# Performance work log

Measured on AMD Instinct MI355X. Metric: run time of the kernel, lower is better.

## Reference

```python
import jax, jax.numpy as jnp
import numpy as np

C = 2.3026  # Poincare ball curvature
EPS = 1e-15

def _hlinear(x, z, r, c):
    # hypll-style Poincare fully connected layer (HNN++, Shimizu et al.)
    # x: (B, fi) on ball, z: (fi, fo), r: (fo,)
    cs = jnp.sqrt(c)
    lam = 2.0 / (1.0 - c * jnp.sum(x * x, axis=-1, keepdims=True))  # conformal factor (B,1)
    zn = jnp.maximum(jnp.sqrt(jnp.sum(z * z, axis=0)), EPS)         # (fo,)
    tcr = 2.0 * cs * r                                              # (fo,)
    # signed hyperplane distances v_k
    d = (2.0 * zn / cs) * jnp.arcsinh(
        cs * lam * (x @ z) / zn * jnp.cosh(tcr) - (lam - 1.0) * jnp.sinh(tcr))
    w = jnp.sinh(cs * d) / cs
    # map back into the ball: ||out|| < 1/sqrt(c)
    return w / (1.0 + jnp.sqrt(1.0 + c * jnp.sum(w * w, axis=-1, keepdims=True)))

def _hrelu(x, c):
    # logmap at origin -> ReLU in tangent space -> expmap at origin
    cs = jnp.sqrt(c)
    n = jnp.maximum(jnp.sqrt(jnp.sum(x * x, axis=-1, keepdims=True)), EPS)
    v = jnp.arctanh(jnp.minimum(cs * n, 1.0 - 1e-7)) * x / (cs * n)
    v = jax.nn.relu(v)
    vn = jnp.maximum(jnp.sqrt(jnp.sum(v * v, axis=-1, keepdims=True)), EPS)
    return jnp.tanh(cs * vn) * v / (cs * vn)

def setup_inputs() -> dict:
    key = jax.random.key(0)
    ks = jax.random.split(key, 9)
    B, D = 65536, 768
    xs = 0.02 * jax.random.normal(ks[0], (B, D), dtype=jnp.float32)
    # repo preprocessing: lift to Lorentz (K=C) then Lorentz->Poincare
    x0 = jnp.sqrt(1.0 / C + jnp.sum(xs * xs, axis=-1, keepdims=True))
    x = xs / (x0 + 1.0)  # strictly inside ball of radius 1/sqrt(C)
    def mk(k, fi, fo):
        return (jax.random.normal(k, (fi, fo), dtype=jnp.float32) / np.float32(np.sqrt(fi)))
    return {
        "x": x,
        "z1": mk(ks[1], 768, 512), "b1": 0.01 * jax.random.normal(ks[2], (512,), dtype=jnp.float32),
        "z2": mk(ks[3], 512, 256), "b2": 0.01 * jax.random.normal(ks[4], (256,), dtype=jnp.float32),
        "z3": mk(ks[5], 256, 128), "b3": 0.01 * jax.random.normal(ks[6], (128,), dtype=jnp.float32),
        "z4": mk(ks[7], 128, 1),   "b4": 0.01 * jax.random.normal(ks[8], (1,), dtype=jnp.float32),
    }

def reference(x, z1, b1, z2, b2, z3, b3, z4, b4):
    h = _hrelu(_hlinear(x, z1, b1, C), C)
    h = _hrelu(_hlinear(h, z2, b2, C), C)
    h = _hrelu(_hlinear(h, z3, b3, C), C)
    return _hlinear(h, z4, b4, C)
```

## Files before the change

### kernel.cpp

```cpp
#include <hip/hip_runtime.h>

#define CURV 2.3026f
#define EPSF 1e-15f

typedef __attribute__((ext_vector_type(8))) short bfrag8;
typedef __attribute__((ext_vector_type(4))) float ffrag4;

__device__ __forceinline__ unsigned short f2bf(float f) {
  unsigned u = __builtin_bit_cast(unsigned, f);
  u += 0x7fffu + ((u >> 16) & 1u);
  return (unsigned short)(u >> 16);
}

__device__ __forceinline__ void gld16(const void* g, void* l) {
  unsigned lo = (unsigned)(unsigned long long)l;
  __builtin_amdgcn_global_load_lds(
      (const __attribute__((address_space(1))) unsigned int*)g,
      (__attribute__((address_space(3))) unsigned int*)lo, 16, 0, 0);
}

__global__ __launch_bounds__(256) void xprep(const float* __restrict__ x,
                                             unsigned short* __restrict__ xb,
                                             float* __restrict__ lam0) {
  const int t = threadIdx.x, lane = t & 63, w = t >> 6;
  const long row = (long)blockIdx.x * 4 + w;
  const float* xr = x + row * 768;
  unsigned short* xo = xb + row * 768;
  float ss = 0.f;
#pragma unroll
  for (int j = 0; j < 3; j++) {
    float4 v = *(const float4*)(xr + 4 * (lane + 64 * j));
    ss += v.x * v.x + v.y * v.y + v.z * v.z + v.w * v.w;
    ushort4 b; b.x = f2bf(v.x); b.y = f2bf(v.y); b.z = f2bf(v.z); b.w = f2bf(v.w);
    *(ushort4*)(xo + 4 * (lane + 64 * j)) = b;
  }
#pragma unroll
  for (int m = 1; m <= 32; m <<= 1) ss += __shfl_xor(ss, m);
  if (lane == 0) lam0[row] = 2.f / (1.f - CURV * ss);
}

__global__ void prep_weights(const float* __restrict__ z, const float* __restrict__ r,
                             unsigned short* __restrict__ zT, float* __restrict__ stats,
                             int K, int N) {
  int n = blockIdx.x, t = threadIdx.x;
  float ss = 0.f;
  for (int k = t; k < K; k += 128) {
    float v = z[(size_t)k * N + n];
    ss += v * v;
    zT[(size_t)n * K + k] = f2bf(v);
  }
  __shared__ float red[128];
  red[t] = ss; __syncthreads();
  for (int s = 64; s > 0; s >>= 1) { if (t < s) red[t] += red[t + s]; __syncthreads(); }
  if (t == 0) {
    float zn = fmaxf(sqrtf(red[0]), EPSF);
    float cs = sqrtf(CURV);
    float tc = 2.f * cs * r[n];
    stats[4*n+0] = 2.f * (zn - 1.f);
    stats[4*n+1] = coshf(tc) / zn;
    stats[4*n+2] = sinhf(tc);
    stats[4*n+3] = 0.f;
  }
}

template<int K, int N, bool LAST>
__launch_bounds__(512, 2)
__global__ void hlayer(const unsigned short* __restrict__ Ain,
                       const unsigned short* __restrict__ zT,
                       const float* __restrict__ stats,
                       const float* __restrict__ lamIn,
                       unsigned short* __restrict__ Hout,
                       float* __restrict__ lamOut,
                       const float* __restrict__ z4,
                       const float* __restrict__ st4,
                       float* __restrict__ outF) {
  constexpr int NT = N / 64;
  constexpr int KI = K / 32;
  constexpr int NBW = N / 128;
  constexpr int BUF = 4096 + N * 64;
  constexpr int HSB = LAST ? 0 : 64 * (N + 8) * 2;
  constexpr int SM = (2 * BUF > HSB) ? 2 * BUF : HSB;
  __shared__ __align__(16) char smem[SM];
  __shared__ float lamS[64];
  __shared__ float gamS[64];
  __shared__ float sums[3][64];

  const int t = threadIdx.x;
  const int wid = t >> 6, lane = t & 63;
  const int wm = wid >> 2, wn = wid & 3;
  const int lm = lane & 15, quad = lane >> 4;
  const int l7 = lane & 7, rl8 = lane >> 3;
  const unsigned rowg0 = blockIdx.x * 64;

  const char* Abase = (const char*)Ain;
  const char* Bbase = (const char*)zT;
  unsigned aoff = 0, aLds = 0;
  if (wid < 4) {
    unsigned R = 8 * wid + rl8;
    unsigned c = l7 ^ rl8;
    unsigned m = 2 * R + (c >> 2);
    aoff = (rowg0 + m) * (unsigned)(K * 2) + (c & 3) * 16;
    aLds = wid * 1024 + lane * 16;
  }
  unsigned boff[NBW], bLds[NBW];
#pragma unroll
  for (int j = 0; j < NBW; j++) {
    unsigned R = 8 * (wid + 8 * j) + rl8;
    unsigned c = l7 ^ rl8;
    unsigned n = 2 * R + (c >> 2);
    boff[j] = n * (unsigned)(K * 2) + (c & 3) * 16;
    bLds[j] = (wid + 8 * j) * 1024 + lane * 16;
  }

  const unsigned sl16 = ((((lm & 1) << 2) + quad) ^ (lm >> 1)) << 4;
  unsigned afoff[2], bfoff[NT];
#pragma unroll
  for (int tm = 0; tm < 2; tm++)
    afoff[tm] = (16 * wm + 8 * tm + (lm >> 1)) * 128 + sl16;
#pragma unroll
  for (int tn = 0; tn < NT; tn++)
    bfoff[tn] = 4096 + (wn * (N / 8) + 8 * tn + (lm >> 1)) * 128 + sl16;

  {
    char* buf = smem;
    if (wid < 4) gld16(Abase + aoff, buf + aLds);
#pragma unroll
    for (int j = 0; j < NBW; j++) gld16(Bbase + boff[j], buf + 4096 + bLds[j]);
  }

  ffrag4 acc[2][NT];
#pragma unroll
  for (int a = 0; a < 2; a++)
#pragma unroll
    for (int b = 0; b < NT; b++) acc[a][b] = (ffrag4){0.f, 0.f, 0.f, 0.f};

  for (int k = 0; k < KI; k++) {
    __syncthreads();
    char* cur = smem + (k & 1) * BUF;
    char* nxt = smem + ((k + 1) & 1) * BUF;
    if (k + 1 < KI) {
      unsigned adv = (unsigned)(k + 1) * 64;
      if (wid < 4) gld16(Abase + aoff + adv, nxt + aLds);
#pragma unroll
      for (int j = 0; j < NBW; j++) gld16(Bbase + boff[j] + adv, nxt + 4096 + bLds[j]);
    }
    bfrag8 af0 = *(const bfrag8*)(cur + afoff[0]);
    bfrag8 af1 = *(const bfrag8*)(cur + afoff[1]);
#pragma unroll
    for (int tn = 0; tn < NT; tn++) {
      bfrag8 bf = *(const bfrag8*)(cur + bfoff[tn]);
      acc[0][tn] = __builtin_amdgcn_mfma_f32_16x16x32_bf16(af0, bf, acc[0][tn], 0, 0, 0);
      acc[1][tn] = __builtin_amdgcn_mfma_f32_16x16x32_bf16(af1, bf, acc[1][tn], 0, 0, 0);
    }
  }

  if (t < 64) {
    sums[0][t] = 0.f; sums[1][t] = 0.f; sums[2][t] = 0.f;
    lamS[t] = lamIn[rowg0 + t];
  }
  float z4v[NT];
  if (LAST) {
#pragma unroll
    for (int tn = 0; tn < NT; tn++) z4v[tn] = z4[wn * (N / 4) + 16 * tn + lm];
  }
  __syncthreads();

  const float cs = sqrtf(CURV), inv_cs = 1.f / cs;

#pragma unroll
  for (int tn = 0; tn < NT; tn++) {
    float4 st = *(const float4*)(stats + 4 * (wn * (N / 4) + 16 * tn + lm));
    float dl = st.x, chozn = st.y, sh = st.z;
#pragma unroll
    for (int tm = 0; tm < 2; tm++) {
#pragma unroll
      for (int rg = 0; rg < 4; rg++) {
        float lam = lamS[32 * wm + 16 * tm + 4 * quad + rg];
        float g = cs * lam * acc[tm][tn][rg] * chozn - (lam - 1.f) * sh;
        float q = g * g;
        float u = g * (1.f - q * (1.f / 6.f) + q * q * 0.075f - q * q * q * 0.044642857f);
        float d1 = dl * u;
        float S = 2.f * g * sqrtf(1.f + q);
        float Ch = 1.f + 2.f * q;
        acc[tm][tn][rg] = (S * (1.f + 0.5f * d1 * d1) + Ch * d1) * inv_cs;
      }
    }
  }
#pragma unroll
  for (int tm = 0; tm < 2; tm++) {
#pragma unroll
    for (int rg = 0; rg < 4; rg++) {
      float s2 = 0.f, sp2 = 0.f, s4 = 0.f;
#pragma unroll
      for (int tn = 0; tn < NT; tn++) {
        float w = acc[tm][tn][rg];
        s2 += w * w;
        float wp = fmaxf(w, 0.f);
        sp2 += wp * wp;
        if (LAST) s4 += wp * z4v[tn];
      }
#pragma unroll
      for (int m = 1; m <= 8; m <<= 1) {
        s2 += __shfl_xor(s2, m, 16);
        sp2 += __shfl_xor(sp2, m, 16);
        if (LAST) s4 += __shfl_xor(s4, m, 16);
      }
      if (lm == 0) {
        int row = 32 * wm + 16 * tm + 4 * quad + rg;
        atomicAdd(&sums[0][row], s2);
        atomicAdd(&sums[1][row], sp2);
        if (LAST) atomicAdd(&sums[2][row], s4);
      }
    }
  }
  __syncthreads();
  if (t < 64) {
    float sw2 = sums[0][t], swp2 = sums[1][t];
    float den = 1.f + sqrtf(1.f + CURV * sw2);
    float nn = fmaxf(sqrtf(sw2) / den, EPSF);
    float al = atanhf(fminf(cs * nn, 1.f - 1e-7f)) / (cs * nn);
    float vn = fmaxf(al * sqrtf(swp2) / den, EPSF);
    float be = tanhf(cs * vn) / (cs * vn);
    float gam = al * be / den;
    if (LAST) {
      float s = gam * sums[2][t];
      float lamh = 2.f / (1.f - CURV * gam * gam * swp2);
      float g = cs * lamh * s * st4[1] - (lamh - 1.f) * st4[2];
      float q = g * g;
      float u = g * (1.f - q * (1.f / 6.f) + q * q * 0.075f - q * q * q * 0.044642857f);
      float d1 = st4[0] * u;
      float S = 2.f * g * sqrtf(1.f + q);
      float Ch = 1.f + 2.f * q;
      float w = (S * (1.f + 0.5f * d1 * d1) + Ch * d1) * inv_cs;
      outF[rowg0 + t] = w / (1.f + sqrtf(1.f + CURV * w * w));
    } else {
      gamS[t] = gam;
      lamOut[rowg0 + t] = 2.f / (1.f - CURV * gam * gam * swp2);
    }
  }
  if (!LAST) {
    __syncthreads();
    unsigned short* HS = (unsigned short*)smem;
#pragma unroll
    for (int tm = 0; tm < 2; tm++)
#pragma unroll
      for (int rg = 0; rg < 4; rg++) {
        int rloc = 32 * wm + 16 * tm + 4 * quad + rg;
        float gam = gamS[rloc];
#pragma unroll
        for (int tn = 0; tn < NT; tn++)
          HS[rloc * (N + 8) + wn * (N / 4) + 16 * tn + lm] = f2bf(gam * fmaxf(acc[tm][tn][rg], 0.f));
      }
    __syncthreads();
    constexpr int NS8 = N / 8;
    constexpr int SL = (8 * N) / 512;
#pragma unroll
    for (int u = 0; u < SL; u++) {
      int sl = t + 512 * u;
      int rl = sl / NS8, cc = sl % NS8;
      uint4 v = *(const uint4*)(HS + rl * (N + 8) + cc * 8);
      *(uint4*)((unsigned short*)Hout + (size_t)(rowg0 + rl) * N + cc * 8) = v;
    }
  }
}

extern "C" void kernel_launch(void* const* d_in, const int* in_sizes, int n_in,
                              void* d_out, int out_size, void* d_ws, size_t ws_size,
                              hipStream_t stream) {
  const float* x  = (const float*)d_in[0];
  const float* z1 = (const float*)d_in[1];
  const float* b1 = (const float*)d_in[2];
  const float* z2 = (const float*)d_in[3];
  const float* b2 = (const float*)d_in[4];
  const float* z3 = (const float*)d_in[5];
  const float* b3 = (const float*)d_in[6];
  const float* z4 = (const float*)d_in[7];
  const float* b4 = (const float*)d_in[8];

  char* ws = (char*)d_ws; size_t off = 0;
  auto carve = [&](size_t b) { char* p = ws + off; off += (b + 255) & ~(size_t)255; return p; };
  unsigned short* zT1 = (unsigned short*)carve(512 * 768 * 2);
  unsigned short* zT2 = (unsigned short*)carve(256 * 512 * 2);
  unsigned short* zT3 = (unsigned short*)carve(128 * 256 * 2);
  unsigned short* zT4 = (unsigned short*)carve(128 * 2);
  float* st1 = (float*)carve(512 * 4 * 4);
  float* st2 = (float*)carve(256 * 4 * 4);
  float* st3 = (float*)carve(128 * 4 * 4);
  float* st4 = (float*)carve(4 * 4);
  float* lam0 = (float*)carve(65536 * 4);
  float* lam1 = (float*)carve(65536 * 4);
  float* lam2 = (float*)carve(65536 * 4);
  unsigned short* xb = (unsigned short*)carve((size_t)65536 * 768 * 2);
  unsigned short* h1 = (unsigned short*)carve((size_t)65536 * 512 * 2);
  unsigned short* h2 = (unsigned short*)carve((size_t)65536 * 256 * 2);

  xprep<<<16384, 256, 0, stream>>>(x, xb, lam0);
  prep_weights<<<512, 128, 0, stream>>>(z1, b1, zT1, st1, 768, 512);
  prep_weights<<<256, 128, 0, stream>>>(z2, b2, zT2, st2, 512, 256);
  prep_weights<<<128, 128, 0, stream>>>(z3, b3, zT3, st3, 256, 128);
  prep_weights<<<1,   128, 0, stream>>>(z4, b4, zT4, st4, 128, 1);

  hlayer<768, 512, false><<<1024, 512, 0, stream>>>(xb, zT1, st1, lam0, h1, lam1, nullptr, nullptr, nullptr);
  hlayer<512, 256, false><<<1024, 512, 0, stream>>>(h1, zT2, st2, lam1, h2, lam2, nullptr, nullptr, nullptr);
  hlayer<256, 128, true ><<<1024, 512, 0, stream>>>(h2, zT3, st3, lam2, nullptr, nullptr, z4, st4, (float*)d_out);
}
```

Measured before the change: 510.5 us.

## Fuse all three hyperbolic layers and x preprocessing into one kernel

Replaces the xprep kernel and three per-layer GEMM kernels with a single 1024-thread kernel that keeps each 64-row block's intermediate activations in shared memory across all layers. The fp32 input is loaded directly to LDS, converted to bf16 in registers, and its row norm is computed on the fly. This removes the global round trips for the bf16 copy of x, h1, h2 and the lambda arrays, plus three launches. In exchange it needs 96KB of LDS per block, which limits occupancy, and weights for layers 2 and 3 are streamed with less overlap.

Measured after the change: 472.4 us. -7.5%, faster.

```diff
diff --git a/kernel.cpp b/kernel.cpp
--- a/kernel.cpp
+++ b/kernel.cpp
@@ -6,37 +6,17 @@
 typedef __attribute__((ext_vector_type(8))) short bfrag8;
 typedef __attribute__((ext_vector_type(4))) float ffrag4;
 
-__device__ __forceinline__ unsigned short f2bf(float f) {
+static __device__ __forceinline__ unsigned short f2bf(float f) {
   unsigned u = __builtin_bit_cast(unsigned, f);
   u += 0x7fffu + ((u >> 16) & 1u);
   return (unsigned short)(u >> 16);
 }
 
-__device__ __forceinline__ void gld16(const void* g, void* l) {
+static __device__ __forceinline__ void gld16(const void* g, void* l) {
   unsigned lo = (unsigned)(unsigned long long)l;
   __builtin_amdgcn_global_load_lds(
       (const __attribute__((address_space(1))) unsigned int*)g,
       (__attribute__((address_space(3))) unsigned int*)lo, 16, 0, 0);
-}
-
-__global__ __launch_bounds__(256) void xprep(const float* __restrict__ x,
-                                             unsigned short* __restrict__ xb,
-                                             float* __restrict__ lam0) {
-  const int t = threadIdx.x, lane = t & 63, w = t >> 6;
-  const long row = (long)blockIdx.x * 4 + w;
-  const float* xr = x + row * 768;
-  unsigned short* xo = xb + row * 768;
-  float ss = 0.f;
-#pragma unroll
-  for (int j = 0; j < 3; j++) {
-    float4 v = *(const float4*)(xr + 4 * (lane + 64 * j));
-    ss += v.x * v.x + v.y * v.y + v.z * v.z + v.w * v.w;
-    ushort4 b; b.x = f2bf(v.x); b.y = f2bf(v.y); b.z = f2bf(v.z); b.w = f2bf(v.w);
-    *(ushort4*)(xo + 4 * (lane + 64 * j)) = b;
-  }
-#pragma unroll
-  for (int m = 1; m <= 32; m <<= 1) ss += __shfl_xor(ss, m);
-  if (lane == 0) lam0[row] = 2.f / (1.f - CURV * ss);
 }
 
 __global__ void prep_weights(const float* __restrict__ z, const float* __restrict__ r,
@@ -63,119 +43,19 @@
   }
 }
 
-template<int K, int N, bool LAST>
-__launch_bounds__(512, 2)
-__global__ void hlayer(const unsigned short* __restrict__ Ain,
-                       const unsigned short* __restrict__ zT,
-                       const float* __restrict__ stats,
-                       const float* __restrict__ lamIn,
-                       unsigned short* __restrict__ Hout,
-                       float* __restrict__ lamOut,
-                       const float* __restrict__ z4,
-                       const float* __restrict__ st4,
-                       float* __restrict__ outF) {
-  constexpr int NT = N / 64;
-  constexpr int KI = K / 32;
-  constexpr int NBW = N / 128;
-  constexpr int BUF = 4096 + N * 64;
-  constexpr int HSB = LAST ? 0 : 64 * (N + 8) * 2;
-  constexpr int SM = (2 * BUF > HSB) ? 2 * BUF : HSB;
-  __shared__ __align__(16) char smem[SM];
-  __shared__ float lamS[64];
-  __shared__ float gamS[64];
-  __shared__ float sums[3][64];
-
-  const int t = threadIdx.x;
-  const int wid = t >> 6, lane = t & 63;
-  const int wm = wid >> 2, wn = wid & 3;
-  const int lm = lane & 15, quad = lane >> 4;
-  const int l7 = lane & 7, rl8 = lane >> 3;
-  const unsigned rowg0 = blockIdx.x * 64;
-
-  const char* Abase = (const char*)Ain;
-  const char* Bbase = (const char*)zT;
-  unsigned aoff = 0, aLds = 0;
-  if (wid < 4) {
-    unsigned R = 8 * wid + rl8;
-    unsigned c = l7 ^ rl8;
-    unsigned m = 2 * R + (c >> 2);
-    aoff = (rowg0 + m) * (unsigned)(K * 2) + (c & 3) * 16;
-    aLds = wid * 1024 + lane * 16;
-  }
-  unsigned boff[NBW], bLds[NBW];
-#pragma unroll
-  for (int j = 0; j < NBW; j++) {
-    unsigned R = 8 * (wid + 8 * j) + rl8;
-    unsigned c = l7 ^ rl8;
-    unsigned n = 2 * R + (c >> 2);
-    boff[j] = n * (unsigned)(K * 2) + (c & 3) * 16;
-    bLds[j] = (wid + 8 * j) * 1024 + lane * 16;
-  }
-
-  const unsigned sl16 = ((((lm & 1) << 2) + quad) ^ (lm >> 1)) << 4;
-  unsigned afoff[2], bfoff[NT];
-#pragma unroll
-  for (int tm = 0; tm < 2; tm++)
-    afoff[tm] = (16 * wm + 8 * tm + (lm >> 1)) * 128 + sl16;
-#pragma unroll
-  for (int tn = 0; tn < NT; tn++)
-    bfoff[tn] = 4096 + (wn * (N / 8) + 8 * tn + (lm >> 1)) * 128 + sl16;
-
-  {
-    char* buf = smem;
-    if (wid < 4) gld16(Abase + aoff, buf + aLds);
-#pragma unroll
-    for (int j = 0; j < NBW; j++) gld16(Bbase + boff[j], buf + 4096 + bLds[j]);
-  }
-
-  ffrag4 acc[2][NT];
-#pragma unroll
-  for (int a = 0; a < 2; a++)
-#pragma unroll
-    for (int b = 0; b < NT; b++) acc[a][b] = (ffrag4){0.f, 0.f, 0.f, 0.f};
-
-  for (int k = 0; k < KI; k++) {
-    __syncthreads();
-    char* cur = smem + (k & 1) * BUF;
-    char* nxt = smem + ((k + 1) & 1) * BUF;
-    if (k + 1 < KI) {
-      unsigned adv = (unsigned)(k + 1) * 64;
-      if (wid < 4) gld16(Abase + aoff + adv, nxt + aLds);
-#pragma unroll
-      for (int j = 0; j < NBW; j++) gld16(Bbase + boff[j] + adv, nxt + 4096 + bLds[j]);
-    }
-    bfrag8 af0 = *(const bfrag8*)(cur + afoff[0]);
-    bfrag8 af1 = *(const bfrag8*)(cur + afoff[1]);
-#pragma unroll
-    for (int tn = 0; tn < NT; tn++) {
-      bfrag8 bf = *(const bfrag8*)(cur + bfoff[tn]);
-      acc[0][tn] = __builtin_amdgcn_mfma_f32_16x16x32_bf16(af0, bf, acc[0][tn], 0, 0, 0);
-      acc[1][tn] = __builtin_amdgcn_mfma_f32_16x16x32_bf16(af1, bf, acc[1][tn], 0, 0, 0);
-    }
-  }
-
-  if (t < 64) {
-    sums[0][t] = 0.f; sums[1][t] = 0.f; sums[2][t] = 0.f;
-    lamS[t] = lamIn[rowg0 + t];
-  }
-  float z4v[NT];
-  if (LAST) {
-#pragma unroll
-    for (int tn = 0; tn < NT; tn++) z4v[tn] = z4[wn * (N / 4) + 16 * tn + lm];
-  }
-  __syncthreads();
-
-  const float cs = sqrtf(CURV), inv_cs = 1.f / cs;
-
+template<int NT>
+static __device__ __forceinline__ void poly_w(ffrag4 (&acc)[2][NT], const float* __restrict__ stats,
+                                              int wn, int lm, int wm, int quad,
+                                              const float* lamP, float cs, float inv_cs) {
 #pragma unroll
   for (int tn = 0; tn < NT; tn++) {
-    float4 st = *(const float4*)(stats + 4 * (wn * (N / 4) + 16 * tn + lm));
+    float4 st = *(const float4*)(stats + 4 * (wn * (16 * NT) + 16 * tn + lm));
     float dl = st.x, chozn = st.y, sh = st.z;
 #pragma unroll
     for (int tm = 0; tm < 2; tm++) {
 #pragma unroll
       for (int rg = 0; rg < 4; rg++) {
-        float lam = lamS[32 * wm + 16 * tm + 4 * quad + rg];
+        float lam = lamP[32 * wm + 16 * tm + 4 * quad + rg];
         float g = cs * lam * acc[tm][tn][rg] * chozn - (lam - 1.f) * sh;
         float q = g * g;
         float u = g * (1.f - q * (1.f / 6.f) + q * q * 0.075f - q * q * q * 0.044642857f);
@@ -186,6 +66,11 @@
       }
     }
   }
+}
+
+template<int NT, bool L4>
+static __device__ __forceinline__ void reduce_rows(ffrag4 (&acc)[2][NT], const float* z4v,
+                                                   int lm, int wm, int quad, float (*sums_)[64]) {
 #pragma unroll
   for (int tm = 0; tm < 2; tm++) {
 #pragma unroll
@@ -197,22 +82,179 @@
         s2 += w * w;
         float wp = fmaxf(w, 0.f);
         sp2 += wp * wp;
-        if (LAST) s4 += wp * z4v[tn];
+        if (L4) s4 += wp * z4v[tn];
       }
 #pragma unroll
       for (int m = 1; m <= 8; m <<= 1) {
         s2 += __shfl_xor(s2, m, 16);
         sp2 += __shfl_xor(sp2, m, 16);
-        if (LAST) s4 += __shfl_xor(s4, m, 16);
+        if (L4) s4 += __shfl_xor(s4, m, 16);
       }
       if (lm == 0) {
         int row = 32 * wm + 16 * tm + 4 * quad + rg;
-        atomicAdd(&sums[0][row], s2);
-        atomicAdd(&sums[1][row], sp2);
-        if (LAST) atomicAdd(&sums[2][row], s4);
-      }
-    }
-  }
+        atomicAdd(&sums_[0][row], s2);
+        atomicAdd(&sums_[1][row], sp2);
+        if (L4) atomicAdd(&sums_[2][row], s4);
+      }
+    }
+  }
+}
+
+template<int NT>
+static __device__ __forceinline__ void panel_write(ffrag4 (&acc)[2][NT], char* panel,
+                                                   int lm, int wm, int wn, int quad,
+                                                   const float* gamP) {
+#pragma unroll
+  for (int tm = 0; tm < 2; tm++)
+#pragma unroll
+    for (int rg = 0; rg < 4; rg++) {
+      const int r = 32 * wm + 16 * tm + 4 * quad + rg;
+      const float gam = gamP[r];
+      const unsigned rb = (unsigned)((r >> 1) * 128);
+      const unsigned rx = (unsigned)((r >> 1) & 7);
+      const unsigned c0 = (unsigned)((r & 1) * 4);
+#pragma unroll
+      for (int tn = 0; tn < NT; tn++) {
+        const int col = wn * (16 * NT) + 16 * tn + lm;
+        const unsigned ad = (unsigned)((col >> 5) * 4096) + rb +
+                            (((c0 + (unsigned)((col >> 3) & 3)) ^ rx) << 4) +
+                            (unsigned)((col & 7) * 2);
+        *(unsigned short*)(panel + ad) = f2bf(gam * fmaxf(acc[tm][tn][rg], 0.f));
+      }
+    }
+}
+
+__launch_bounds__(1024, 4)
+__global__ void fused_mlp(const float* __restrict__ x,
+                          const unsigned short* __restrict__ zt1, const float* __restrict__ st1,
+                          const unsigned short* __restrict__ zt2, const float* __restrict__ st2,
+                          const unsigned short* __restrict__ zt3, const float* __restrict__ st3,
+                          const float* __restrict__ z4, const float* __restrict__ st4,
+                          float* __restrict__ outF) {
+  __shared__ __align__(16) char smem[98304];
+  __shared__ float lamS[64];
+  __shared__ float gamS[64];
+  __shared__ float sums[3][64];
+
+  const int t = threadIdx.x;
+  const int wid = t >> 6, lane = t & 63;
+  const int wm = wid >> 3, wn = wid & 7;
+  const int lm = lane & 15, quad = lane >> 4;
+  const int l7 = lane & 7, rl8 = lane >> 3;
+  const unsigned rowg0 = blockIdx.x * 64u;
+
+  char* const A1 = smem;
+  char* const B1 = smem + 16384;
+  char* const H1 = smem;
+  char* const B2 = smem + 65536;
+  char* const H2 = smem + 65536;
+  char* const B3 = smem;
+
+  const unsigned cA = (unsigned)(l7 ^ rl8);
+  const unsigned ldst = (unsigned)(lane * 16);
+
+  const unsigned sl16 = (unsigned)(((((lm & 1) << 2) + quad) ^ (lm >> 1)) << 4);
+  unsigned afoff[2];
+#pragma unroll
+  for (int tm = 0; tm < 2; tm++) afoff[tm] = (unsigned)((16 * wm + 8 * tm + (lm >> 1)) * 128) + sl16;
+  unsigned a32off[2][2];
+#pragma unroll
+  for (int tm = 0; tm < 2; tm++) {
+    int r = 32 * wm + 16 * tm + lm;
+#pragma unroll
+    for (int j = 0; j < 2; j++)
+      a32off[tm][j] = (unsigned)(r * 128 + (((2 * quad + j) ^ (r & 7)) * 16));
+  }
+  unsigned bf1off[4];
+#pragma unroll
+  for (int tn = 0; tn < 4; tn++) bf1off[tn] = (unsigned)((wn * 32 + 8 * tn + (lm >> 1)) * 128) + sl16;
+  unsigned bf2off[2];
+#pragma unroll
+  for (int tn = 0; tn < 2; tn++) bf2off[tn] = (unsigned)((wn * 16 + 8 * tn + (lm >> 1)) * 128) + sl16;
+  const unsigned bf3off = (unsigned)((wn * 8 + (lm >> 1)) * 128) + sl16;
+
+  unsigned a1src = 0;
+  if (wid < 8) a1src = (rowg0 + 8u * (unsigned)wid + (unsigned)rl8) * 3072u + cA * 16u;
+  const unsigned a1dst = (unsigned)(wid * 1024) + ldst;
+  unsigned b1src[2], b1dst[2];
+#pragma unroll
+  for (int j = 0; j < 2; j++) {
+    unsigned R = (unsigned)(8 * (wid + 16 * j) + rl8);
+    unsigned n = 2u * R + (cA >> 2);
+    b1src[j] = n * 1536u + (cA & 3u) * 16u;
+    b1dst[j] = (unsigned)((wid + 16 * j) * 1024) + ldst;
+  }
+  const unsigned R2 = (unsigned)(8 * wid + rl8);
+  const unsigned b2src = (2u * R2 + (cA >> 2)) * 1024u + (cA & 3u) * 16u;
+  const unsigned b2dst = (unsigned)(wid * 1024) + ldst;
+  const unsigned b3src = (2u * R2 + (cA >> 2)) * 512u + (cA & 3u) * 16u;
+
+  if (wid < 8) gld16((const char*)x + a1src, A1 + a1dst);
+  gld16((const char*)zt1 + b1src[0], B1 + b1dst[0]);
+  gld16((const char*)zt1 + b1src[1], B1 + b1dst[1]);
+
+  ffrag4 acc1[2][4];
+#pragma unroll
+  for (int a = 0; a < 2; a++)
+#pragma unroll
+    for (int b = 0; b < 4; b++) acc1[a][b] = (ffrag4){0.f, 0.f, 0.f, 0.f};
+  float ss0 = 0.f, ss1 = 0.f;
+
+  for (int k = 0; k < 24; k++) {
+    __syncthreads();
+    char* curA = A1 + (k & 1) * 8192;
+    char* curB = B1 + (k & 1) * 32768;
+    if (k + 1 < 24) {
+      char* nA = A1 + ((k + 1) & 1) * 8192;
+      char* nB = B1 + ((k + 1) & 1) * 32768;
+      unsigned advA = (unsigned)(k + 1) * 128u;
+      unsigned advB = (unsigned)(k + 1) * 64u;
+      if (wid < 8) gld16((const char*)x + a1src + advA, nA + a1dst);
+      gld16((const char*)zt1 + b1src[0] + advB, nB + b1dst[0]);
+      gld16((const char*)zt1 + b1src[1] + advB, nB + b1dst[1]);
+    }
+    bfrag8 af[2];
+#pragma unroll
+    for (int tm = 0; tm < 2; tm++) {
+      float4 fa = *(const float4*)(curA + a32off[tm][0]);
+      float4 fb = *(const float4*)(curA + a32off[tm][1]);
+      if (wn == 0) {
+        float s = fa.x * fa.x + fa.y * fa.y + fa.z * fa.z + fa.w * fa.w
+                + fb.x * fb.x + fb.y * fb.y + fb.z * fb.z + fb.w * fb.w;
+        if (tm == 0) ss0 += s; else ss1 += s;
+      }
+      bfrag8 v;
+      v[0] = (short)f2bf(fa.x); v[1] = (short)f2bf(fa.y);
+      v[2] = (short)f2bf(fa.z); v[3] = (short)f2bf(fa.w);
+      v[4] = (short)f2bf(fb.x); v[5] = (short)f2bf(fb.y);
+      v[6] = (short)f2bf(fb.z); v[7] = (short)f2bf(fb.w);
+      af[tm] = v;
+    }
+#pragma unroll
+    for (int tn = 0; tn < 4; tn++) {
+      bfrag8 bf = *(const bfrag8*)(curB + bf1off[tn]);
+      acc1[0][tn] = __builtin_amdgcn_mfma_f32_16x16x32_bf16(af[0], bf, acc1[0][tn], 0, 0, 0);
+      acc1[1][tn] = __builtin_amdgcn_mfma_f32_16x16x32_bf16(af[1], bf, acc1[1][tn], 0, 0, 0);
+    }
+  }
+
+  if (wn == 0) {
+    ss0 += __shfl_xor(ss0, 16); ss0 += __shfl_xor(ss0, 32);
+    ss1 += __shfl_xor(ss1, 16); ss1 += __shfl_xor(ss1, 32);
+    if (quad == 0) {
+      lamS[32 * wm + lm]      = 2.f / (1.f - CURV * ss0);
+      lamS[32 * wm + 16 + lm] = 2.f / (1.f - CURV * ss1);
+    }
+  }
+  if (t < 64) { sums[0][t] = 0.f; sums[1][t] = 0.f; }
+  __syncthreads();
+
+  gld16((const char*)zt2 + b2src, B2 + b2dst);
+  gld16((const char*)zt2 + b2src + 64u, B2 + 16384 + b2dst);
+
+  const float cs = sqrtf(CURV), inv_cs = 1.f / cs;
+  poly_w<4>(acc1, st1, wn, lm, wm, quad, lamS, cs, inv_cs);
+  reduce_rows<4, false>(acc1, nullptr, lm, wm, quad, sums);
   __syncthreads();
   if (t < 64) {
     float sw2 = sums[0][t], swp2 = sums[1][t];
@@ -222,45 +264,98 @@
     float vn = fmaxf(al * sqrtf(swp2) / den, EPSF);
     float be = tanhf(cs * vn) / (cs * vn);
     float gam = al * be / den;
-    if (LAST) {
-      float s = gam * sums[2][t];
-      float lamh = 2.f / (1.f - CURV * gam * gam * swp2);
-      float g = cs * lamh * s * st4[1] - (lamh - 1.f) * st4[2];
-      float q = g * g;
-      float u = g * (1.f - q * (1.f / 6.f) + q * q * 0.075f - q * q * q * 0.044642857f);
-      float d1 = st4[0] * u;
-      float S = 2.f * g * sqrtf(1.f + q);
-      float Ch = 1.f + 2.f * q;
-      float w = (S * (1.f + 0.5f * d1 * d1) + Ch * d1) * inv_cs;
-      outF[rowg0 + t] = w / (1.f + sqrtf(1.f + CURV * w * w));
-    } else {
-      gamS[t] = gam;
-      lamOut[rowg0 + t] = 2.f / (1.f - CURV * gam * gam * swp2);
-    }
-  }
-  if (!LAST) {
+    gamS[t] = gam;
+    lamS[t] = 2.f / (1.f - CURV * gam * gam * swp2);
+  }
+  __syncthreads();
+  panel_write<4>(acc1, H1, lm, wm, wn, quad, gamS);
+
+  ffrag4 acc2[2][2];
+#pragma unroll
+  for (int a = 0; a < 2; a++)
+#pragma unroll
+    for (int b = 0; b < 2; b++) acc2[a][b] = (ffrag4){0.f, 0.f, 0.f, 0.f};
+  if (t < 64) { sums[0][t] = 0.f; sums[1][t] = 0.f; }
+
+  for (int k = 0; k < 16; k++) {
     __syncthreads();
-    unsigned short* HS = (unsigned short*)smem;
-#pragma unroll
-    for (int tm = 0; tm < 2; tm++)
-#pragma unroll
-      for (int rg = 0; rg < 4; rg++) {
-        int rloc = 32 * wm + 16 * tm + 4 * quad + rg;
-        float gam = gamS[rloc];
-#pragma unroll
-        for (int tn = 0; tn < NT; tn++)
-          HS[rloc * (N + 8) + wn * (N / 4) + 16 * tn + lm] = f2bf(gam * fmaxf(acc[tm][tn][rg], 0.f));
-      }
+    char* curB = B2 + (k & 1) * 16384;
+    if (k > 0 && k + 1 < 16)
+      gld16((const char*)zt2 + b2src + (unsigned)(k + 1) * 64u,
+            B2 + ((k + 1) & 1) * 16384 + b2dst);
+    bfrag8 a0 = *(const bfrag8*)(H1 + k * 4096 + afoff[0]);
+    bfrag8 a1 = *(const bfrag8*)(H1 + k * 4096 + afoff[1]);
+#pragma unroll
+    for (int tn = 0; tn < 2; tn++) {
+      bfrag8 bf = *(const bfrag8*)(curB + bf2off[tn]);
+      acc2[0][tn] = __builtin_amdgcn_mfma_f32_16x16x32_bf16(a0, bf, acc2[0][tn], 0, 0, 0);
+      acc2[1][tn] = __builtin_amdgcn_mfma_f32_16x16x32_bf16(a1, bf, acc2[1][tn], 0, 0, 0);
+    }
+  }
+  __syncthreads();
+
+  if (wid < 8) {
+    gld16((const char*)zt3 + b3src, B3 + b2dst);
+    gld16((const char*)zt3 + b3src + 64u, B3 + 8192 + b2dst);
+  }
+  poly_w<2>(acc2, st2, wn, lm, wm, quad, lamS, cs, inv_cs);
+  reduce_rows<2, false>(acc2, nullptr, lm, wm, quad, sums);
+  __syncthreads();
+  if (t < 64) {
+    float sw2 = sums[0][t], swp2 = sums[1][t];
+    float den = 1.f + sqrtf(1.f + CURV * sw2);
+    float nn = fmaxf(sqrtf(sw2) / den, EPSF);
+    float al = atanhf(fminf(cs * nn, 1.f - 1e-7f)) / (cs * nn);
+    float vn = fmaxf(al * sqrtf(swp2) / den, EPSF);
+    float be = tanhf(cs * vn) / (cs * vn);
+    float gam = al * be / den;
+    gamS[t] = gam;
+    lamS[t] = 2.f / (1.f - CURV * gam * gam * swp2);
+  }
+  __syncthreads();
+  panel_write<2>(acc2, H2, lm, wm, wn, quad, gamS);
+
+  ffrag4 acc3[2][1];
+  acc3[0][0] = (ffrag4){0.f, 0.f, 0.f, 0.f};
+  acc3[1][0] = (ffrag4){0.f, 0.f, 0.f, 0.f};
+  if (t < 64) { sums[0][t] = 0.f; sums[1][t] = 0.f; sums[2][t] = 0.f; }
+  float z4v[1] = { z4[wn * 16 + lm] };
+
+  for (int k = 0; k < 8; k++) {
     __syncthreads();
-    constexpr int NS8 = N / 8;
-    constexpr int SL = (8 * N) / 512;
-#pragma unroll
-    for (int u = 0; u < SL; u++) {
-      int sl = t + 512 * u;
-      int rl = sl / NS8, cc = sl % NS8;
-      uint4 v = *(const uint4*)(HS + rl * (N + 8) + cc * 8);
-      *(uint4*)((unsigned short*)Hout + (size_t)(rowg0 + rl) * N + cc * 8) = v;
-    }
+    char* curB = B3 + (k & 1) * 8192;
+    if (k > 0 && k + 1 < 8 && wid < 8)
+      gld16((const char*)zt3 + b3src + (unsigned)(k + 1) * 64u,
+            B3 + ((k + 1) & 1) * 8192 + b2dst);
+    bfrag8 a0 = *(const bfrag8*)(H2 + k * 4096 + afoff[0]);
+    bfrag8 a1 = *(const bfrag8*)(H2 + k * 4096 + afoff[1]);
+    bfrag8 bf = *(const bfrag8*)(curB + bf3off);
+    acc3[0][0] = __builtin_amdgcn_mfma_f32_16x16x32_bf16(a0, bf, acc3[0][0], 0, 0, 0);
+    acc3[1][0] = __builtin_amdgcn_mfma_f32_16x16x32_bf16(a1, bf, acc3[1][0], 0, 0, 0);
+  }
+  __syncthreads();
+
+  poly_w<1>(acc3, st3, wn, lm, wm, quad, lamS, cs, inv_cs);
+  reduce_rows<1, true>(acc3, z4v, lm, wm, quad, sums);
+  __syncthreads();
+  if (t < 64) {
+    float sw2 = sums[0][t], swp2 = sums[1][t];
+    float den = 1.f + sqrtf(1.f + CURV * sw2);
+    float nn = fmaxf(sqrtf(sw2) / den, EPSF);
+    float al = atanhf(fminf(cs * nn, 1.f - 1e-7f)) / (cs * nn);
+    float vn = fmaxf(al * sqrtf(swp2) / den, EPSF);
+    float be = tanhf(cs * vn) / (cs * vn);
+    float gam = al * be / den;
+    float s = gam * sums[2][t];
+    float lamh = 2.f / (1.f - CURV * gam * gam * swp2);
+    float g = cs * lamh * s * st4[1] - (lamh - 1.f) * st4[2];
+    float q = g * g;
+    float u = g * (1.f - q * (1.f / 6.f) + q * q * 0.075f - q * q * q * 0.044642857f);
+    float d1 = st4[0] * u;
+    float S = 2.f * g * sqrtf(1.f + q);
+    float Ch = 1.f + 2.f * q;
+    float w = (S * (1.f + 0.5f * d1 * d1) + Ch * d1) * inv_cs;
+    outF[rowg0 + t] = w / (1.f + sqrtf(1.f + CURV * w * w));
   }
 }
 
@@ -287,20 +382,11 @@
   float* st2 = (float*)carve(256 * 4 * 4);
   float* st3 = (float*)carve(128 * 4 * 4);
   float* st4 = (float*)carve(4 * 4);
-  float* lam0 = (float*)carve(65536 * 4);
-  float* lam1 = (float*)carve(65536 * 4);
-  float* lam2 = (float*)carve(65536 * 4);
-  unsigned short* xb = (unsigned short*)carve((size_t)65536 * 768 * 2);
-  unsigned short* h1 = (unsigned short*)carve((size_t)65536 * 512 * 2);
-  unsigned short* h2 = (unsigned short*)carve((size_t)65536 * 256 * 2);
-
-  xprep<<<16384, 256, 0, stream>>>(x, xb, lam0);
+
   prep_weights<<<512, 128, 0, stream>>>(z1, b1, zT1, st1, 768, 512);
   prep_weights<<<256, 128, 0, stream>>>(z2, b2, zT2, st2, 512, 256);
   prep_weights<<<128, 128, 0, stream>>>(z3, b3, zT3, st3, 256, 128);
   prep_weights<<<1,   128, 0, stream>>>(z4, b4, zT4, st4, 128, 1);
 
-  hlayer<768, 512, false><<<1024, 512, 0, stream>>>(xb, zT1, st1, lam0, h1, lam1, nullptr, nullptr, nullptr);
-  hlayer<512, 256, false><<<1024, 512, 0, stream>>>(h1, zT2, st2, lam1, h2, lam2, nullptr, nullptr, nullptr);
-  hlayer<256, 128, true ><<<1024, 512, 0, stream>>>(h2, zT3, st3, lam2, nullptr, nullptr, z4, st4, (float*)d_out);
-}
+  fused_mlp<<<1024, 1024, 0, stream>>>(x, zT1, st1, zT2, st2, zT3, st3, z4, st4, (float*)d_out);
+}
```
